# Performance work log

Hardware: AMD Instinct MI355X
Metric: run time of the kernel (lower is better)

## Reference

```python
import jax, jax.numpy as jnp
import numpy as np

DROP_SCALE = 1e-4  # tf.multiply(feat_dropout, 0.0001)


def setup_inputs() -> dict:
    key = jax.random.key(0)
    k1, k2 = jax.random.split(key)
    B, C, N, D = 128, 2, 256, 256
    x = jax.random.normal(k1, (B, C, N, D), dtype=jnp.float32)
    # glorot_uniform for kernel [C*N*D, N]
    fan_in, fan_out = C * N * D, N
    limit = np.sqrt(6.0 / (fan_in + fan_out)).astype(np.float32)
    W = jax.random.uniform(k2, (fan_in, fan_out), dtype=jnp.float32,
                           minval=-limit, maxval=limit)
    return {"x": x, "W": W}


def _forward(x, W):
    B, C, N, D = x.shape
    K = N // 2  # with continuous data, exactly half strictly exceed the median
    # Keras Flatten(channels_first): permute to channels-last order, then flatten
    xf = jnp.transpose(x, (0, 2, 3, 1)).reshape(B, -1)          # [B, N*D*C]
    line = jax.nn.sigmoid(xf @ W)                                # [B, N]
    med = jnp.median(line, axis=-1, keepdims=True)               # [B, 1]
    mask = med < line                                            # [B, N] bool
    mask3 = jnp.broadcast_to(mask[:, None, :], (B, C, N))        # tile over channels
    # ragged boolean_mask + to_tensor == stable compaction of kept rows.
    # Stable argsort of (~mask) puts True (kept) positions first, in order.
    idx_att = jnp.argsort(~mask3, axis=-1, stable=True)[..., :K]   # [B, C, K]
    idx_drp = jnp.argsort(mask3, axis=-1, stable=True)[..., :K]    # [B, C, K]
    feat_att = jnp.take_along_axis(x, idx_att[..., None], axis=2)  # [B, C, K, D]
    feat_drp = jnp.take_along_axis(x, idx_drp[..., None], axis=2)  # [B, C, K, D]
    return feat_att + DROP_SCALE * feat_drp


def reference(x, W):
    return _forward(x, W)
```

## Files before the change

### kernel.cpp

```cpp
#include <hip/hip_runtime.h>

#define BATCH 128
#define CH    2
#define NN    256
#define DD    256
#define KTOT  131072
#define KHALF 128

#define KSPLIT 256
#define KLEN   (KTOT / KSPLIT)
#define KS     32
#define NSTAGE (KLEN / KS)

typedef short bf16x8 __attribute__((ext_vector_type(8)));
typedef float f32x4  __attribute__((ext_vector_type(4)));

__device__ __forceinline__ unsigned int bf16_rne(float f) {
    unsigned int u = __float_as_uint(f);
    return (u + 0x7FFFu + ((u >> 16) & 1u)) >> 16;
}
__device__ __forceinline__ float bf16f(unsigned int h) {
    return __uint_as_float(h << 16);
}

template <bool ATOMIC>
__global__ __launch_bounds__(512, 2) void gemm_mfma(const float* __restrict__ x,
                                                    const float* __restrict__ W,
                                                    float* __restrict__ zout) {
    __shared__ unsigned short Ah[128][40], Al[128][40];
    __shared__ unsigned short Bh[256][40], Bl[256][40];

    const int t  = threadIdx.x;
    const int k0 = blockIdx.x * KLEN;
    const int c  = k0 >> 16;
    const int nd_base = k0 & 65535;

    const int tb = t >> 2;
    const int tk = (t & 3) * 8;
    const int ti = (t >> 6) * 4;
    const int tj = (t & 63) * 4;

    float4 xa0, xa1, wb0, wb1, wb2, wb3;

    auto load_stage = [&](int s) {
        const size_t kk = (size_t)k0 + s * KS;
        xa0 = *(const float4*)&x[(size_t)tb * KTOT + kk + tk];
        xa1 = *(const float4*)&x[(size_t)tb * KTOT + kk + tk + 4];
        const int nd0 = nd_base + s * KS + ti;
        wb0 = *(const float4*)&W[(size_t)(2 * (nd0 + 0) + c) * NN + tj];
        wb1 = *(const float4*)&W[(size_t)(2 * (nd0 + 1) + c) * NN + tj];
        wb2 = *(const float4*)&W[(size_t)(2 * (nd0 + 2) + c) * NN + tj];
        wb3 = *(const float4*)&W[(size_t)(2 * (nd0 + 3) + c) * NN + tj];
    };

    auto write_stage = [&]() {
        float v[8] = {xa0.x, xa0.y, xa0.z, xa0.w, xa1.x, xa1.y, xa1.z, xa1.w};
        unsigned int h[8], l[8];
#pragma unroll
        for (int i = 0; i < 8; ++i) {
            h[i] = bf16_rne(v[i]);
            l[i] = bf16_rne(v[i] - bf16f(h[i]));
        }
        uint4 ph, pl;
        ph.x = h[0] | (h[1] << 16); ph.y = h[2] | (h[3] << 16);
        ph.z = h[4] | (h[5] << 16); ph.w = h[6] | (h[7] << 16);
        pl.x = l[0] | (l[1] << 16); pl.y = l[2] | (l[3] << 16);
        pl.z = l[4] | (l[5] << 16); pl.w = l[6] | (l[7] << 16);
        *(uint4*)&Ah[tb][tk] = ph;
        *(uint4*)&Al[tb][tk] = pl;

        const float* r0 = (const float*)&wb0;
        const float* r1 = (const float*)&wb1;
        const float* r2 = (const float*)&wb2;
        const float* r3 = (const float*)&wb3;
#pragma unroll
        for (int cc = 0; cc < 4; ++cc) {
            float w0 = r0[cc], w1 = r1[cc], w2 = r2[cc], w3 = r3[cc];
            unsigned int h0 = bf16_rne(w0), h1 = bf16_rne(w1),
                         h2 = bf16_rne(w2), h3 = bf16_rne(w3);
            unsigned int l0 = bf16_rne(w0 - bf16f(h0)), l1 = bf16_rne(w1 - bf16f(h1)),
                         l2 = bf16_rne(w2 - bf16f(h2)), l3 = bf16_rne(w3 - bf16f(h3));
            uint2 qh, ql;
            qh.x = h0 | (h1 << 16); qh.y = h2 | (h3 << 16);
            ql.x = l0 | (l1 << 16); ql.y = l2 | (l3 << 16);
            *(uint2*)&Bh[tj + cc][ti] = qh;
            *(uint2*)&Bl[tj + cc][ti] = ql;
        }
    };

    const int lane = t & 63;
    const int wv   = t >> 6;
    const int wm   = (wv >> 2) * 64;
    const int wn   = (wv & 3) * 64;
    const int lr   = lane & 15;
    const int kh   = (lane >> 4) * 8;

    f32x4 acc[4][4] = {};

    auto compute_stage = [&]() {
        bf16x8 a_h[4], a_l[4];
#pragma unroll
        for (int mt = 0; mt < 4; ++mt) {
            a_h[mt] = *(const bf16x8*)&Ah[wm + mt * 16 + lr][kh];
            a_l[mt] = *(const bf16x8*)&Al[wm + mt * 16 + lr][kh];
        }
#pragma unroll
        for (int nt = 0; nt < 4; ++nt) {
            bf16x8 b_h = *(const bf16x8*)&Bh[wn + nt * 16 + lr][kh];
            bf16x8 b_l = *(const bf16x8*)&Bl[wn + nt * 16 + lr][kh];
#pragma unroll
            for (int mt = 0; mt < 4; ++mt) {
                acc[mt][nt] = __builtin_amdgcn_mfma_f32_16x16x32_bf16(a_h[mt], b_h, acc[mt][nt], 0, 0, 0);
                acc[mt][nt] = __builtin_amdgcn_mfma_f32_16x16x32_bf16(a_h[mt], b_l, acc[mt][nt], 0, 0, 0);
                acc[mt][nt] = __builtin_amdgcn_mfma_f32_16x16x32_bf16(a_l[mt], b_h, acc[mt][nt], 0, 0, 0);
            }
        }
    };

    load_stage(0);
    for (int s = 0; s < NSTAGE; ++s) {
        __syncthreads();
        write_stage();
        __syncthreads();
        if (s + 1 < NSTAGE) load_stage(s + 1);
        compute_stage();
    }

#pragma unroll
    for (int mt = 0; mt < 4; ++mt)
#pragma unroll
        for (int nt = 0; nt < 4; ++nt)
#pragma unroll
            for (int r = 0; r < 4; ++r) {
                const int row = wm + mt * 16 + (lane >> 4) * 4 + r;
                const int col = wn + nt * 16 + lr;
                if (ATOMIC) atomicAdd(&zout[row * NN + col], acc[mt][nt][r]);
                else zout[(size_t)blockIdx.x * (BATCH * NN) + row * NN + col] = acc[mt][nt][r];
            }
}

__global__ __launch_bounds__(256) void reduce_select(const float* __restrict__ part, int nsplit,
                                                     int* __restrict__ idx_att,
                                                     int* __restrict__ idx_drp) {
    __shared__ float zv[NN];
    __shared__ int   flags[NN];
    const int b = blockIdx.x;
    const int j = threadIdx.x;
    float v = 0.0f;
    for (int s = 0; s < nsplit; ++s)
        v += part[(size_t)s * (BATCH * NN) + b * NN + j];
    zv[j] = v;
    __syncthreads();
    int rank = 0;
    for (int i = 0; i < NN; ++i) {
        const float u = zv[i];
        rank += (u < v) || (u == v && i < j);
    }
    const int kept = (rank >= KHALF) ? 1 : 0;
    flags[j] = kept;
    __syncthreads();
    int pos = 0;
    for (int i = 0; i < j; ++i) pos += flags[i];
    if (kept) idx_att[b * KHALF + pos]       = j;
    else      idx_drp[b * KHALF + (j - pos)] = j;
}

__global__ __launch_bounds__(256) void gather_kernel(const float* __restrict__ x,
                                                     const int* __restrict__ idx_att,
                                                     const int* __restrict__ idx_drp,
                                                     float* __restrict__ out) {
    const int row  = blockIdx.x * 4 + (threadIdx.x >> 6);
    const int lane = threadIdx.x & 63;
    const int k = row & 127;
    const int c = (row >> 7) & 1;
    const int b = row >> 8;
    const int ia = idx_att[b * KHALF + k];
    const int id = idx_drp[b * KHALF + k];
    const float4* pa = (const float4*)&x[((b * 2 + c) * NN + ia) * DD];
    const float4* pd = (const float4*)&x[((b * 2 + c) * NN + id) * DD];
    float4* po = (float4*)&out[(size_t)row * DD];
    const float4 a  = pa[lane];
    const float4 d4 = pd[lane];
    float4 o;
    o.x = a.x + 1e-4f * d4.x;
    o.y = a.y + 1e-4f * d4.y;
    o.z = a.z + 1e-4f * d4.z;
    o.w = a.w + 1e-4f * d4.w;
    po[lane] = o;
}

extern "C" void kernel_launch(void* const* d_in, const int* in_sizes, int n_in,
                              void* d_out, int out_size, void* d_ws, size_t ws_size,
                              hipStream_t stream) {
    const float* x = (const float*)d_in[0];
    const float* W = (const float*)d_in[1];
    float* out = (float*)d_out;

    const size_t partial_bytes = (size_t)KSPLIT * BATCH * NN * sizeof(float);
    const size_t idx_bytes = (size_t)BATCH * KHALF * sizeof(int);

    if (ws_size >= partial_bytes + 2 * idx_bytes) {
        float* part    = (float*)d_ws;
        int*   idx_att = (int*)((char*)d_ws + partial_bytes);
        int*   idx_drp = idx_att + BATCH * KHALF;
        gemm_mfma<false><<<KSPLIT, 512, 0, stream>>>(x, W, part);
        reduce_select<<<BATCH, 256, 0, stream>>>(part, KSPLIT, idx_att, idx_drp);
        gather_kernel<<<BATCH * CH * KHALF / 4, 256, 0, stream>>>(x, idx_att, idx_drp, out);
    } else {
        float* z       = (float*)d_ws;
        int*   idx_att = (int*)((char*)d_ws + (size_t)BATCH * NN * sizeof(float));
        int*   idx_drp = idx_att + BATCH * KHALF;
        hipMemsetAsync(z, 0, BATCH * NN * sizeof(float), stream);
        gemm_mfma<true><<<KSPLIT, 512, 0, stream>>>(x, W, z);
        reduce_select<<<BATCH, 256, 0, stream>>>(z, 1, idx_att, idx_drp);
        gather_kernel<<<BATCH * CH * KHALF / 4, 256, 0, stream>>>(x, idx_att, idx_drp, out);
    }
}
```

Baseline: 327.2 us.

## Split GEMM N across two blocks and parallelize split-K reduction

The GEMM now runs as 512 blocks of 256 threads. Each block covers half of the output columns for one K slice, and block IDs are interleaved so the paired halves run close together and share the x reads. Staging loads are restructured so each thread loads 16 contiguous x floats and 16 W values down a column. The serial 256-way partial-sum reduction inside the select kernel is replaced by a 1024-block reduce1 pass down to 8 partials, followed by a lighter select. This adds more blocks and an extra launch in exchange for better occupancy and a much less serialized reduction, but the x tile is now loaded twice and the W loads are strided.

```diff
diff --git a/kernel.cpp b/kernel.cpp
--- a/kernel.cpp
+++ b/kernel.cpp
@@ -11,89 +11,93 @@
 #define KLEN   (KTOT / KSPLIT)
 #define KS     32
 #define NSTAGE (KLEN / KS)
+#define NTB    128
+#define PITCH  40
 
 typedef short bf16x8 __attribute__((ext_vector_type(8)));
 typedef float f32x4  __attribute__((ext_vector_type(4)));
 
-__device__ __forceinline__ unsigned int bf16_rne(float f) {
+__device__ __forceinline__ unsigned short bf16_rne(float f) {
     unsigned int u = __float_as_uint(f);
-    return (u + 0x7FFFu + ((u >> 16) & 1u)) >> 16;
-}
-__device__ __forceinline__ float bf16f(unsigned int h) {
-    return __uint_as_float(h << 16);
+    u += 0x7FFFu + ((u >> 16) & 1u);
+    return (unsigned short)(u >> 16);
+}
+__device__ __forceinline__ float bf16f(unsigned short h) {
+    return __uint_as_float(((unsigned int)h) << 16);
+}
+__device__ __forceinline__ uint4 pack8(const unsigned short* p) {
+    uint4 r;
+    r.x = (unsigned)p[0] | ((unsigned)p[1] << 16);
+    r.y = (unsigned)p[2] | ((unsigned)p[3] << 16);
+    r.z = (unsigned)p[4] | ((unsigned)p[5] << 16);
+    r.w = (unsigned)p[6] | ((unsigned)p[7] << 16);
+    return r;
 }
 
 template <bool ATOMIC>
-__global__ __launch_bounds__(512, 2) void gemm_mfma(const float* __restrict__ x,
+__global__ __launch_bounds__(256, 2) void gemm_mfma(const float* __restrict__ x,
                                                     const float* __restrict__ W,
                                                     float* __restrict__ zout) {
-    __shared__ unsigned short Ah[128][40], Al[128][40];
-    __shared__ unsigned short Bh[256][40], Bl[256][40];
+    __shared__ unsigned short Ah[128][PITCH], Al[128][PITCH];
+    __shared__ unsigned short Bh[NTB][PITCH], Bl[NTB][PITCH];
+
+    const int bid = blockIdx.x;
+    const int s   = ((bid >> 4) << 3) | (bid & 7);
+    const int nh  = (bid >> 3) & 1;
 
     const int t  = threadIdx.x;
-    const int k0 = blockIdx.x * KLEN;
+    const int k0 = s * KLEN;
     const int c  = k0 >> 16;
     const int nd_base = k0 & 65535;
 
-    const int tb = t >> 2;
-    const int tk = (t & 3) * 8;
-    const int ti = (t >> 6) * 4;
-    const int tj = (t & 63) * 4;
-
-    float4 xa0, xa1, wb0, wb1, wb2, wb3;
-
-    auto load_stage = [&](int s) {
-        const size_t kk = (size_t)k0 + s * KS;
-        xa0 = *(const float4*)&x[(size_t)tb * KTOT + kk + tk];
-        xa1 = *(const float4*)&x[(size_t)tb * KTOT + kk + tk + 4];
-        const int nd0 = nd_base + s * KS + ti;
-        wb0 = *(const float4*)&W[(size_t)(2 * (nd0 + 0) + c) * NN + tj];
-        wb1 = *(const float4*)&W[(size_t)(2 * (nd0 + 1) + c) * NN + tj];
-        wb2 = *(const float4*)&W[(size_t)(2 * (nd0 + 2) + c) * NN + tj];
-        wb3 = *(const float4*)&W[(size_t)(2 * (nd0 + 3) + c) * NN + tj];
+    const int ra = t & 127;
+    const int ha = t >> 7;
+    const int cb = t & 127;
+    const int hb = t >> 7;
+
+    float av[16], bv[16];
+
+    auto load_stage = [&](int st) {
+        const float* xp = &x[(size_t)ra * KTOT + k0 + st * KS + 16 * ha];
+        *(float4*)&av[0]  = *(const float4*)&xp[0];
+        *(float4*)&av[4]  = *(const float4*)&xp[4];
+        *(float4*)&av[8]  = *(const float4*)&xp[8];
+        *(float4*)&av[12] = *(const float4*)&xp[12];
+        const int nd0 = nd_base + st * KS + 16 * hb;
+        const float* wp = &W[(size_t)(2 * nd0 + c) * NN + nh * NTB + cb];
+#pragma unroll
+        for (int i = 0; i < 16; ++i)
+            bv[i] = wp[(size_t)i * 2 * NN];
     };
 
     auto write_stage = [&]() {
-        float v[8] = {xa0.x, xa0.y, xa0.z, xa0.w, xa1.x, xa1.y, xa1.z, xa1.w};
-        unsigned int h[8], l[8];
-#pragma unroll
-        for (int i = 0; i < 8; ++i) {
-            h[i] = bf16_rne(v[i]);
-            l[i] = bf16_rne(v[i] - bf16f(h[i]));
-        }
-        uint4 ph, pl;
-        ph.x = h[0] | (h[1] << 16); ph.y = h[2] | (h[3] << 16);
-        ph.z = h[4] | (h[5] << 16); ph.w = h[6] | (h[7] << 16);
-        pl.x = l[0] | (l[1] << 16); pl.y = l[2] | (l[3] << 16);
-        pl.z = l[4] | (l[5] << 16); pl.w = l[6] | (l[7] << 16);
-        *(uint4*)&Ah[tb][tk] = ph;
-        *(uint4*)&Al[tb][tk] = pl;
-
-        const float* r0 = (const float*)&wb0;
-        const float* r1 = (const float*)&wb1;
-        const float* r2 = (const float*)&wb2;
-        const float* r3 = (const float*)&wb3;
-#pragma unroll
-        for (int cc = 0; cc < 4; ++cc) {
-            float w0 = r0[cc], w1 = r1[cc], w2 = r2[cc], w3 = r3[cc];
-            unsigned int h0 = bf16_rne(w0), h1 = bf16_rne(w1),
-                         h2 = bf16_rne(w2), h3 = bf16_rne(w3);
-            unsigned int l0 = bf16_rne(w0 - bf16f(h0)), l1 = bf16_rne(w1 - bf16f(h1)),
-                         l2 = bf16_rne(w2 - bf16f(h2)), l3 = bf16_rne(w3 - bf16f(h3));
-            uint2 qh, ql;
-            qh.x = h0 | (h1 << 16); qh.y = h2 | (h3 << 16);
-            ql.x = l0 | (l1 << 16); ql.y = l2 | (l3 << 16);
-            *(uint2*)&Bh[tj + cc][ti] = qh;
-            *(uint2*)&Bl[tj + cc][ti] = ql;
-        }
+        unsigned short h[16], l[16];
+#pragma unroll
+        for (int i = 0; i < 16; ++i) {
+            h[i] = bf16_rne(av[i]);
+            l[i] = bf16_rne(av[i] - bf16f(h[i]));
+        }
+        *(uint4*)&Ah[ra][16 * ha]     = pack8(h);
+        *(uint4*)&Ah[ra][16 * ha + 8] = pack8(h + 8);
+        *(uint4*)&Al[ra][16 * ha]     = pack8(l);
+        *(uint4*)&Al[ra][16 * ha + 8] = pack8(l + 8);
+#pragma unroll
+        for (int i = 0; i < 16; ++i) {
+            h[i] = bf16_rne(bv[i]);
+            l[i] = bf16_rne(bv[i] - bf16f(h[i]));
+        }
+        *(uint4*)&Bh[cb][16 * hb]     = pack8(h);
+        *(uint4*)&Bh[cb][16 * hb + 8] = pack8(h + 8);
+        *(uint4*)&Bl[cb][16 * hb]     = pack8(l);
+        *(uint4*)&Bl[cb][16 * hb + 8] = pack8(l + 8);
     };
 
     const int lane = t & 63;
-    const int wv   = t >> 6;
-    const int wm   = (wv >> 2) * 64;
-    const int wn   = (wv & 3) * 64;
+    const int wid  = t >> 6;
+    const int wm   = (wid >> 1) * 64;
+    const int wn   = (wid & 1) * 64;
     const int lr   = lane & 15;
-    const int kh   = (lane >> 4) * 8;
+    const int kq   = (lane >> 4) * 8;
 
     f32x4 acc[4][4] = {};
 
@@ -101,13 +105,13 @@
         bf16x8 a_h[4], a_l[4];
 #pragma unroll
         for (int mt = 0; mt < 4; ++mt) {
-            a_h[mt] = *(const bf16x8*)&Ah[wm + mt * 16 + lr][kh];
-            a_l[mt] = *(const bf16x8*)&Al[wm + mt * 16 + lr][kh];
+            a_h[mt] = *(const bf16x8*)&Ah[wm + mt * 16 + lr][kq];
+            a_l[mt] = *(const bf16x8*)&Al[wm + mt * 16 + lr][kq];
         }
 #pragma unroll
         for (int nt = 0; nt < 4; ++nt) {
-            bf16x8 b_h = *(const bf16x8*)&Bh[wn + nt * 16 + lr][kh];
-            bf16x8 b_l = *(const bf16x8*)&Bl[wn + nt * 16 + lr][kh];
+            bf16x8 b_h = *(const bf16x8*)&Bh[wn + nt * 16 + lr][kq];
+            bf16x8 b_l = *(const bf16x8*)&Bl[wn + nt * 16 + lr][kq];
 #pragma unroll
             for (int mt = 0; mt < 4; ++mt) {
                 acc[mt][nt] = __builtin_amdgcn_mfma_f32_16x16x32_bf16(a_h[mt], b_h, acc[mt][nt], 0, 0, 0);
@@ -118,11 +122,11 @@
     };
 
     load_stage(0);
-    for (int s = 0; s < NSTAGE; ++s) {
+    for (int st = 0; st < NSTAGE; ++st) {
         __syncthreads();
         write_stage();
         __syncthreads();
-        if (s + 1 < NSTAGE) load_stage(s + 1);
+        if (st + 1 < NSTAGE) load_stage(st + 1);
         compute_stage();
     }
 
@@ -133,13 +137,25 @@
 #pragma unroll
             for (int r = 0; r < 4; ++r) {
                 const int row = wm + mt * 16 + (lane >> 4) * 4 + r;
-                const int col = wn + nt * 16 + lr;
+                const int col = nh * NTB + wn + nt * 16 + lr;
                 if (ATOMIC) atomicAdd(&zout[row * NN + col], acc[mt][nt][r]);
-                else zout[(size_t)blockIdx.x * (BATCH * NN) + row * NN + col] = acc[mt][nt][r];
+                else zout[(size_t)s * (BATCH * NN) + row * NN + col] = acc[mt][nt][r];
             }
 }
 
-__global__ __launch_bounds__(256) void reduce_select(const float* __restrict__ part, int nsplit,
+__global__ __launch_bounds__(256) void reduce1(const float* __restrict__ part,
+                                               float* __restrict__ part2) {
+    const int g = blockIdx.x & 7;
+    const int b = blockIdx.x >> 3;
+    const int j = threadIdx.x;
+    float v = 0.0f;
+#pragma unroll
+    for (int i = 0; i < 32; ++i)
+        v += part[(size_t)(g * 32 + i) * (BATCH * NN) + b * NN + j];
+    part2[(size_t)g * (BATCH * NN) + b * NN + j] = v;
+}
+
+__global__ __launch_bounds__(256) void select_kernel(const float* __restrict__ p2, int ngroups,
                                                      int* __restrict__ idx_att,
                                                      int* __restrict__ idx_drp) {
     __shared__ float zv[NN];
@@ -147,8 +163,8 @@
     const int b = blockIdx.x;
     const int j = threadIdx.x;
     float v = 0.0f;
-    for (int s = 0; s < nsplit; ++s)
-        v += part[(size_t)s * (BATCH * NN) + b * NN + j];
+    for (int g = 0; g < ngroups; ++g)
+        v += p2[(size_t)g * (BATCH * NN) + b * NN + j];
     zv[j] = v;
     __syncthreads();
     int rank = 0;
@@ -196,23 +212,26 @@
     const float* W = (const float*)d_in[1];
     float* out = (float*)d_out;
 
-    const size_t partial_bytes = (size_t)KSPLIT * BATCH * NN * sizeof(float);
-    const size_t idx_bytes = (size_t)BATCH * KHALF * sizeof(int);
-
-    if (ws_size >= partial_bytes + 2 * idx_bytes) {
+    const size_t part_bytes  = (size_t)KSPLIT * BATCH * NN * sizeof(float);
+    const size_t part2_bytes = (size_t)8 * BATCH * NN * sizeof(float);
+    const size_t idx_bytes   = (size_t)BATCH * KHALF * sizeof(int);
+
+    if (ws_size >= part_bytes + part2_bytes + 2 * idx_bytes) {
         float* part    = (float*)d_ws;
-        int*   idx_att = (int*)((char*)d_ws + partial_bytes);
+        float* part2   = (float*)((char*)d_ws + part_bytes);
+        int*   idx_att = (int*)((char*)d_ws + part_bytes + part2_bytes);
         int*   idx_drp = idx_att + BATCH * KHALF;
-        gemm_mfma<false><<<KSPLIT, 512, 0, stream>>>(x, W, part);
-        reduce_select<<<BATCH, 256, 0, stream>>>(part, KSPLIT, idx_att, idx_drp);
+        gemm_mfma<false><<<512, 256, 0, stream>>>(x, W, part);
+        reduce1<<<1024, 256, 0, stream>>>(part, part2);
+        select_kernel<<<BATCH, 256, 0, stream>>>(part2, 8, idx_att, idx_drp);
         gather_kernel<<<BATCH * CH * KHALF / 4, 256, 0, stream>>>(x, idx_att, idx_drp, out);
     } else {
         float* z       = (float*)d_ws;
         int*   idx_att = (int*)((char*)d_ws + (size_t)BATCH * NN * sizeof(float));
         int*   idx_drp = idx_att + BATCH * KHALF;
-        hipMemsetAsync(z, 0, BATCH * NN * sizeof(float), stream);
-        gemm_mfma<true><<<KSPLIT, 512, 0, stream>>>(x, W, z);
-        reduce_select<<<BATCH, 256, 0, stream>>>(z, 1, idx_att, idx_drp);
+        hipMemsetAsync(z, 0, (size_t)BATCH * NN * sizeof(float), stream);
+        gemm_mfma<true><<<512, 256, 0, stream>>>(x, W, z);
+        select_kernel<<<BATCH, 256, 0, stream>>>(z, 1, idx_att, idx_drp);
         gather_kernel<<<BATCH * CH * KHALF / 4, 256, 0, stream>>>(x, idx_att, idx_drp, out);
     }
 }
```

Result: faster. 274.6 us (-16.1%).
